# Optimization experiments

Measured on AMD Instinct MI355X. Metric: run time of the kernel, lower is better.

## Reference

```python
import jax, jax.numpy as jnp
import numpy as np

NEG_INF = -1e9

def setup_inputs() -> dict:
    key = jax.random.key(0)
    ks = jax.random.split(key, 7)
    B, NQ, NK, DQ, DK, DV, DH = 16, 128, 2048, 256, 256, 128, 64
    queries = jax.random.normal(ks[0], (B, NQ, DQ), dtype=jnp.float32)
    keys = jax.random.normal(ks[1], (B, NK, DK), dtype=jnp.float32)
    values = jax.random.normal(ks[2], (B, NK, DV), dtype=jnp.float32)
    valid_lens = jax.random.randint(ks[3], (B,), 1, NK + 1, dtype=jnp.int32)
    Wq = jax.random.normal(ks[4], (DQ, DH), dtype=jnp.float32) / np.sqrt(DQ)
    Wk = jax.random.normal(ks[5], (DK, DH), dtype=jnp.float32) / np.sqrt(DK)
    wv = jax.random.normal(ks[6], (DH,), dtype=jnp.float32) / np.sqrt(DH)
    return {"queries": queries, "keys": keys, "values": values,
            "valid_lens": valid_lens, "Wq": Wq, "Wk": Wk, "wv": wv}


def reference(queries, keys, values, valid_lens, Wq, Wk, wv):
    # Additive (Bahdanau) attention.
    q = jnp.einsum('bqd,dh->bqh', queries, Wq)   # [B, nq, dH]
    k = jnp.einsum('bkd,dh->bkh', keys, Wk)      # [B, nk, dH]
    # broadcast add -> tanh -> reduce with wv: scores [B, nq, nk]
    feat = jnp.tanh(q[:, :, None, :] + k[:, None, :, :])  # [B, nq, nk, dH]
    scores = jnp.einsum('bqkh,h->bqk', feat, wv)
    # masked softmax over nk using per-batch valid lengths
    nk = keys.shape[1]
    mask = jnp.arange(nk)[None, None, :] < valid_lens[:, None, None]  # [B,1,nk]
    scores = jnp.where(mask, scores, NEG_INF)
    attn = jax.nn.softmax(scores, axis=-1)
    # dropout is identity at eval time
    return jnp.einsum('bqk,bkv->bqv', attn, values)  # [B, nq, dv]
```

## Files before the change

### kernel.cpp

```cpp
#include <hip/hip_runtime.h>
#include <stddef.h>


__device__ __forceinline__ float fast_rcp(float x)  { return __builtin_amdgcn_rcpf(x); }
__device__ __forceinline__ float fast_exp2(float x) { return __builtin_amdgcn_exp2f(x); }

#define C2F 2.88539008177792681f
#define L2E 1.44269504088896340f

template<int MODE>
__device__ __forceinline__
void proj_body(const float* __restrict__ inb, const float* __restrict__ W,
               float* __restrict__ out, int b, int r0, int rowsPerB, int t)
{
  __shared__ float4 Wlds[256 * 16];
  __shared__ float  klds[64 * 36];

  const float4* W4 = (const float4*)W;
  #pragma unroll
  for (int i = 0; i < 16; ++i) Wlds[t + 256 * i] = W4[t + 256 * i];

  const int j = t >> 4;
  const int g = t & 15;

  float acc[4][4];
  #pragma unroll
  for (int m = 0; m < 4; ++m)
    acc[m][0] = acc[m][1] = acc[m][2] = acc[m][3] = 0.f;

  for (int dc = 0; dc < 8; ++dc) {
    {
      const int row = t >> 2, cs = (t & 3) * 8;
      const float* s = inb + row * 256 + dc * 32 + cs;
      float4 a0 = *(const float4*)s;
      float4 a1 = *(const float4*)(s + 4);
      float* dst = &klds[row * 36 + cs];
      *(float4*)dst       = a0;
      *(float4*)(dst + 4) = a1;
    }
    __syncthreads();
    #pragma unroll
    for (int d = 0; d < 32; ++d) {
      float4 w4 = Wlds[(dc * 32 + d) * 16 + j];
      #pragma unroll
      for (int m = 0; m < 4; ++m) {
        float kv = klds[(g + 16 * m) * 36 + d];
        acc[m][0] = fmaf(kv, w4.x, acc[m][0]);
        acc[m][1] = fmaf(kv, w4.y, acc[m][1]);
        acc[m][2] = fmaf(kv, w4.z, acc[m][2]);
        acc[m][3] = fmaf(kv, w4.w, acc[m][3]);
      }
    }
    __syncthreads();
  }

  if constexpr (MODE == 1) {
    #pragma unroll
    for (int m = 0; m < 4; ++m) {
      int k = r0 + g + 16 * m;
      size_t base = ((size_t)(b * 16 + (k >> 7)) * 64) * 128 + (k & 127);
      #pragma unroll
      for (int i = 0; i < 4; ++i)
        out[base + (size_t)(4 * j + i) * 128] = fast_exp2(C2F * acc[m][i]);
    }
  } else if constexpr (MODE == 2) {
    #pragma unroll
    for (int m = 0; m < 4; ++m) {
      int k = r0 + g + 16 * m;
      size_t base = (size_t)(b * 16 + (k >> 7)) * 8192 + (size_t)(k & 127) * 2;
      float e0 = fast_exp2(C2F * acc[m][0]);
      float e1 = fast_exp2(C2F * acc[m][1]);
      float e2 = fast_exp2(C2F * acc[m][2]);
      float e3 = fast_exp2(C2F * acc[m][3]);
      *(float2*)&out[base + (size_t)(2 * j) * 256]     = make_float2(e0, e1);
      *(float2*)&out[base + (size_t)(2 * j + 1) * 256] = make_float2(e2, e3);
    }
  } else {
    #pragma unroll
    for (int m = 0; m < 4; ++m) {
      int row = r0 + g + 16 * m;
      float4 o;
      o.x = fast_exp2(C2F * acc[m][0]);
      o.y = fast_exp2(C2F * acc[m][1]);
      o.z = fast_exp2(C2F * acc[m][2]);
      o.w = fast_exp2(C2F * acc[m][3]);
      *(float4*)&out[((size_t)b * rowsPerB + row) * 64 + 4 * j] = o;
    }
  }
}

__global__ __launch_bounds__(256)
void proj_qk_kernel(const float* __restrict__ queries, const float* __restrict__ keys,
                    const float* __restrict__ Wq, const float* __restrict__ Wk,
                    float* __restrict__ Eq, float* __restrict__ EkP,
                    const int* __restrict__ vlens)
{
  const int blk = blockIdx.x;
  if (blk >= 512) {
    const int idx = blk - 512;
    const int b = idx & 15, rt = idx >> 4, r0 = rt * 64;
    proj_body<0>(queries + ((size_t)b * 128 + r0) * 256, Wq, Eq, b, r0, 128,
                 threadIdx.x);
  } else {
    const int b = blk & 15, rt = blk >> 4, r0 = rt * 64;
    if (r0 >= vlens[b]) return;
    proj_body<2>(keys + ((size_t)b * 2048 + r0) * 256, Wk, EkP, b, r0, 2048,
                 threadIdx.x);
  }
}

template<int MODE, bool CHECK>
__global__ __launch_bounds__(256)
void proj_kernel(const float* __restrict__ in, const float* __restrict__ W,
                 float* __restrict__ out, const int* __restrict__ vlens,
                 int rowsPerB)
{
  const int t  = threadIdx.x;
  const int b  = blockIdx.x & 15;
  const int rt = blockIdx.x >> 4;
  const int r0 = rt * 64;
  if constexpr (CHECK) {
    if (r0 >= vlens[b]) return;
  }
  proj_body<MODE>(in + ((size_t)b * rowsPerB + r0) * 256, W, out, b, r0,
                  rowsPerB, t);
}

__global__ __launch_bounds__(512, 6)
void scorepv_kernel(const float* __restrict__ Eq, const float* __restrict__ EkP,
                    const float* __restrict__ values, const int* __restrict__ vlens,
                    const float* __restrict__ wv,
                    float* __restrict__ partial, float* __restrict__ tsum)
{
  const int blk = blockIdx.x;
  const int g   = blk >> 3;
  const int qq  = blk & 7;
  const int kt  = g >> 4;
  const int b   = g & 15;
  const int vl  = vlens[b];
  if (kt * 128 >= vl) return;

  __shared__ float ek_lds[64 * 128];

  const int t = threadIdx.x;

  {
    const float4* src = (const float4*)(EkP + (size_t)(b * 16 + kt) * 8192);
    float4* dst = (float4*)ek_lds;
    #pragma unroll
    for (int i = 0; i < 4; ++i) dst[t + 512 * i] = src[t + 512 * i];
  }

  float w0 = 0.f, W1 = 0.f;
  #pragma unroll
  for (int u = 0; u < 16; ++u) {
    float4 v = ((const float4*)wv)[u];
    w0 += v.x + v.y + v.z + v.w;
    W1 += fabsf(v.x) + fabsf(v.y) + fabsf(v.z) + fabsf(v.w);
  }

  __syncthreads();

  const int wave_u = __builtin_amdgcn_readfirstlane(t >> 6);
  const int lane   = t & 63;
  const int q0g    = qq * 16 + wave_u * 2;
  const int kp     = lane * 2;
  const float* eqb = Eq + (size_t)(b * 128 + q0g) * 64;

  float s[2][2] = {{w0, w0}, {w0, w0}};

  const float4* ek4 = (const float4*)ek_lds;
  #pragma unroll 8
  for (int hp = 0; hp < 32; ++hp) {
    float4 e = ek4[hp * 64 + lane];
    float2 wvp = *(const float2*)&wv[2 * hp];
    float wa = -2.0f * wvp.x, wb = -2.0f * wvp.y;
    #pragma unroll
    for (int q = 0; q < 2; ++q) {
      float2 eqp = *(const float2*)&eqb[q * 64 + 2 * hp];
      { float x0 = fmaf(eqp.x, e.x, 1.f), x1 = fmaf(eqp.y, e.y, 1.f);
        float y = fast_rcp(x0 * x1);
        float a = wb * x0; a = fmaf(wa, x1, a);
        s[q][0] = fmaf(a, y, s[q][0]); }
      { float x0 = fmaf(eqp.x, e.z, 1.f), x1 = fmaf(eqp.y, e.w, 1.f);
        float y = fast_rcp(x0 * x1);
        float a = wb * x0; a = fmaf(wa, x1, a);
        s[q][1] = fmaf(a, y, s[q][1]); }
    }
  }

  const int kbase = kt * 128 + kp;
  float p[2][2];
  #pragma unroll
  for (int q = 0; q < 2; ++q) {
    p[q][0] = (kbase     < vl) ? fast_exp2((s[q][0] - W1) * L2E) : 0.f;
    p[q][1] = (kbase + 1 < vl) ? fast_exp2((s[q][1] - W1) * L2E) : 0.f;
  }

  #pragma unroll
  for (int q = 0; q < 2; ++q) {
    float e = p[q][0] + p[q][1];
    #pragma unroll
    for (int m = 1; m < 64; m <<= 1) e += __shfl_xor(e, m, 64);
    if (lane == 0) tsum[(size_t)(b * 16 + kt) * 128 + q0g + q] = e;
  }

  __syncthreads();
  float* p_lds = ek_lds;
  const int q0l = wave_u * 2;
  *(float2*)&p_lds[kp * 20 + q0l]       = make_float2(p[0][0], p[1][0]);
  *(float2*)&p_lds[(kp + 1) * 20 + q0l] = make_float2(p[0][1], p[1][1]);
  __syncthreads();

  const int kg = t >> 7, v = t & 127;
  const int kloc = min(128, vl - kt * 128);
  const int k0 = kg * 32, k1 = min(k0 + 32, kloc);
  const int len = (k1 > k0) ? (k1 - k0) : 0;
  const int nfull = len & ~7;
  const float* vb = values + ((size_t)(b * 2048 + kt * 128)) * 128 + v;
  float acc[16];
  #pragma unroll
  for (int i = 0; i < 16; ++i) acc[i] = 0.f;

  for (int kb = k0; kb < k0 + nfull; kb += 8) {
    float vv[8];
    #pragma unroll
    for (int j = 0; j < 8; ++j) vv[j] = vb[(size_t)(kb + j) * 128];
    #pragma unroll
    for (int j = 0; j < 8; ++j) {
      const float* pr = &p_lds[(kb + j) * 20];
      float4 p0 = *(const float4*)&pr[0];
      float4 p1 = *(const float4*)&pr[4];
      float4 p2 = *(const float4*)&pr[8];
      float4 p3 = *(const float4*)&pr[12];
      float vx = vv[j];
      acc[ 0]=fmaf(p0.x,vx,acc[ 0]); acc[ 1]=fmaf(p0.y,vx,acc[ 1]);
      acc[ 2]=fmaf(p0.z,vx,acc[ 2]); acc[ 3]=fmaf(p0.w,vx,acc[ 3]);
      acc[ 4]=fmaf(p1.x,vx,acc[ 4]); acc[ 5]=fmaf(p1.y,vx,acc[ 5]);
      acc[ 6]=fmaf(p1.z,vx,acc[ 6]); acc[ 7]=fmaf(p1.w,vx,acc[ 7]);
      acc[ 8]=fmaf(p2.x,vx,acc[ 8]); acc[ 9]=fmaf(p2.y,vx,acc[ 9]);
      acc[10]=fmaf(p2.z,vx,acc[10]); acc[11]=fmaf(p2.w,vx,acc[11]);
      acc[12]=fmaf(p3.x,vx,acc[12]); acc[13]=fmaf(p3.y,vx,acc[13]);
      acc[14]=fmaf(p3.z,vx,acc[14]); acc[15]=fmaf(p3.w,vx,acc[15]);
    }
  }
  for (int k = k0 + nfull; k < k1; ++k) {
    float vx = vb[(size_t)k * 128];
    const float* pr = &p_lds[k * 20];
    #pragma unroll
    for (int q = 0; q < 16; ++q) acc[q] = fmaf(pr[q], vx, acc[q]);
  }

  __syncthreads();
  float* red = ek_lds;
  if (kg > 0) {
    #pragma unroll
    for (int q = 0; q < 16; ++q) red[(kg - 1) * 2048 + q * 128 + v] = acc[q];
  }
  __syncthreads();
  if (kg == 0) {
    #pragma unroll
    for (int q = 0; q < 16; ++q) {
      float tot = acc[q] + red[q * 128 + v] + red[2048 + q * 128 + v]
                + red[4096 + q * 128 + v];
      partial[(((size_t)(b * 128 + qq * 16 + q)) * 16 + kt) * 128 + v] = tot;
    }
  }
}

__global__ __launch_bounds__(256)
void reduce_kernel(const float* __restrict__ partial, const float* __restrict__ tsum,
                   const int* __restrict__ vlens, float* __restrict__ out)
{
  const int blk = blockIdx.x;
  const int b   = blk >> 6;
  const int q   = (blk & 63) * 2 + (threadIdx.x >> 7);
  const int v   = threadIdx.x & 127;
  const int ntk = (vlens[b] + 127) >> 7;

  float tot = 0.f;
  for (int i = 0; i < ntk; ++i)
    tot += tsum[(size_t)(b * 16 + i) * 128 + q];

  float acc = 0.f;
  const float* pp = partial + ((size_t)(b * 128 + q)) * 16 * 128 + v;
  for (int i = 0; i < ntk; ++i)
    acc += pp[(size_t)i * 128];

  out[((size_t)(b * 128 + q)) * 128 + v] = acc / tot;
}

__global__ __launch_bounds__(256)
void attn_kernel(const float* __restrict__ Eq, const float* __restrict__ EkT,
                 const float* __restrict__ values, const int* __restrict__ vlens,
                 const float* __restrict__ wv, float* __restrict__ out)
{
  const int t    = threadIdx.x;
  const int b    = blockIdx.x & 15;
  const int qt   = blockIdx.x >> 4;
  const int wave = t >> 6;
  const int lane = t & 63;

  __shared__ float4 sc4[512 * 4];
  __shared__ float  pvp[128 * 5];
  __shared__ float  linvs[4];

  const int vl = vlens[b];

  float eqv[64], wv2[64];
  float w0 = 0.f;
  {
    const float4* eq4 = (const float4*)(Eq + (size_t)(b * 128 + qt * 4 + wave) * 64);
    const float4* wv4 = (const float4*)wv;
    #pragma unroll
    for (int u = 0; u < 16; ++u) {
      float4 e = eq4[u], v = wv4[u];
      eqv[4*u+0] = e.x; eqv[4*u+1] = e.y; eqv[4*u+2] = e.z; eqv[4*u+3] = e.w;
      wv2[4*u+0] = -2.f * v.x; wv2[4*u+1] = -2.f * v.y;
      wv2[4*u+2] = -2.f * v.z; wv2[4*u+3] = -2.f * v.w;
      w0 += v.x + v.y + v.z + v.w;
    }
  }

  const int ktiles = (vl + 127) >> 7;
  const int kp = 2 * lane;
  for (int kt = 0; kt < ktiles; ++kt) {
    const float* tb = EkT + ((size_t)(b * 16 + kt) * 64) * 128 + kp;
    float s0 = w0, s1 = w0;
    #pragma unroll
    for (int h = 0; h < 64; ++h) {
      float2 ek = *(const float2*)(tb + (size_t)h * 128);
      float r0 = fast_rcp(fmaf(eqv[h], ek.x, 1.0f));
      float r1 = fast_rcp(fmaf(eqv[h], ek.y, 1.0f));
      s0 = fmaf(wv2[h], r0, s0);
      s1 = fmaf(wv2[h], r1, s1);
    }
    int k = kt * 128 + kp;
    if (k     >= vl) s0 = -1e9f;
    if (k + 1 >= vl) s1 = -1e9f;
    float* scf = (float*)sc4;
    *(float2*)(scf + (((k >> 2) * 4 + wave) * 4 + (k & 3))) = make_float2(s0, s1);
  }

  const int nq4 = (vl + 3) >> 2;
  float mx = -3e38f;
  for (int Q = lane; Q < nq4; Q += 64) {
    float4 f = sc4[Q * 4 + wave];
    mx = fmaxf(mx, fmaxf(fmaxf(f.x, f.y), fmaxf(f.z, f.w)));
  }
  #pragma unroll
  for (int msk = 1; msk < 64; msk <<= 1) mx = fmaxf(mx, __shfl_xor(mx, msk, 64));
  float lsum = 0.f;
  for (int Q = lane; Q < nq4; Q += 64) {
    float4 f = sc4[Q * 4 + wave];
    f.x = fast_exp2((f.x - mx) * L2E);
    f.y = fast_exp2((f.y - mx) * L2E);
    f.z = fast_exp2((f.z - mx) * L2E);
    f.w = fast_exp2((f.w - mx) * L2E);
    sc4[Q * 4 + wave] = f;
    lsum += f.x + f.y + f.z + f.w;
  }
  #pragma unroll
  for (int msk = 1; msk < 64; msk <<= 1) lsum += __shfl_xor(lsum, msk, 64);
  if (lane == 0) linvs[wave] = fast_rcp(lsum);
  __syncthreads();

  const int grp = t >> 7, v = t & 127;
  float acc[4] = {0.f, 0.f, 0.f, 0.f};
  const float* vb = values + (size_t)b * 2048 * 128 + v;
  for (int Q = grp; Q < nq4; Q += 2) {
    float4 p0 = sc4[Q * 4 + 0], p1 = sc4[Q * 4 + 1];
    float4 p2 = sc4[Q * 4 + 2], p3 = sc4[Q * 4 + 3];
    const float* vk = vb + (size_t)(Q * 4) * 128;
    float x;
    x = vk[0];
    acc[0]=fmaf(p0.x,x,acc[0]); acc[1]=fmaf(p1.x,x,acc[1]);
    acc[2]=fmaf(p2.x,x,acc[2]); acc[3]=fmaf(p3.x,x,acc[3]);
    x = vk[128];
    acc[0]=fmaf(p0.y,x,acc[0]); acc[1]=fmaf(p1.y,x,acc[1]);
    acc[2]=fmaf(p2.y,x,acc[2]); acc[3]=fmaf(p3.y,x,acc[3]);
    x = vk[256];
    acc[0]=fmaf(p0.z,x,acc[0]); acc[1]=fmaf(p1.z,x,acc[1]);
    acc[2]=fmaf(p2.z,x,acc[2]); acc[3]=fmaf(p3.z,x,acc[3]);
    x = vk[384];
    acc[0]=fmaf(p0.w,x,acc[0]); acc[1]=fmaf(p1.w,x,acc[1]);
    acc[2]=fmaf(p2.w,x,acc[2]); acc[3]=fmaf(p3.w,x,acc[3]);
  }
  if (grp == 1) {
    #pragma unroll
    for (int qq = 0; qq < 4; ++qq) pvp[v * 5 + qq] = acc[qq];
  }
  __syncthreads();
  if (grp == 0) {
    #pragma unroll
    for (int qq = 0; qq < 4; ++qq) {
      float tot = acc[qq] + pvp[v * 5 + qq];
      out[((size_t)(b * 128) + qt * 4 + qq) * 128 + v] = tot * linvs[qq];
    }
  }
}

extern "C" void kernel_launch(void* const* d_in, const int* in_sizes, int n_in,
                              void* d_out, int out_size, void* d_ws, size_t ws_size,
                              hipStream_t stream) {
  const float* queries = (const float*)d_in[0];
  const float* keys    = (const float*)d_in[1];
  const float* values  = (const float*)d_in[2];
  const int*   vlens   = (const int*)d_in[3];
  const float* Wq      = (const float*)d_in[4];
  const float* Wk      = (const float*)d_in[5];
  const float* wv      = (const float*)d_in[6];
  float* outp = (float*)d_out;

  float* base    = (float*)d_ws;
  float* Eq      = base;
  float* EkP     = base + 131072;
  float* tsumb   = base + 2228224;
  float* partial = base + 2260992;
  const size_t need = (size_t)(2260992 + 4194304) * 4;

  if (ws_size >= need) {
    hipLaunchKernelGGL(proj_qk_kernel, dim3(544), dim3(256), 0, stream,
                       queries, keys, Wq, Wk, Eq, EkP, vlens);
    hipLaunchKernelGGL(scorepv_kernel, dim3(2048), dim3(512), 0, stream,
                       Eq, EkP, values, vlens, wv, partial, tsumb);
    hipLaunchKernelGGL(reduce_kernel, dim3(1024), dim3(256), 0, stream,
                       partial, tsumb, vlens, outp);
  } else {
    hipLaunchKernelGGL((proj_kernel<0, false>), dim3(32), dim3(256), 0, stream,
                       queries, Wq, Eq, (const int*)nullptr, 128);
    hipLaunchKernelGGL((proj_kernel<1, true>), dim3(512), dim3(256), 0, stream,
                       keys, Wk, EkP, vlens, 2048);
    hipLaunchKernelGGL(attn_kernel, dim3(512), dim3(256), 0, stream,
                       Eq, EkP, values, vlens, wv, outp);
  }
}
```

Measured before the change: 91.24 us.

## Use persistent blocks with atomic work queue over valid tiles only

Adds an init kernel that builds prefix sums of per-batch valid tile counts and resets atomic counters. The projection and score/PV kernels become persistent loops that pull compacted work units from an atomic counter, so no blocks are launched only to exit on masked tiles. The score kernel's launch bounds occupancy hint is raised from 6 to 8. This costs an extra tiny kernel launch, per-unit atomics and barriers, and a linear batch search per unit.

```diff
diff --git a/kernel.cpp b/kernel.cpp
--- a/kernel.cpp
+++ b/kernel.cpp
@@ -7,6 +7,32 @@
 
 #define C2F 2.88539008177792681f
 #define L2E 1.44269504088896340f
+
+#define M_CNTP 0
+#define M_CNTS 1
+#define M_NP   2
+#define M_NS   3
+#define M_PPK  8
+#define M_PSC  32
+
+__global__ void init_kernel(const int* __restrict__ vlens, int* __restrict__ meta)
+{
+  if (threadIdx.x == 0) {
+    int ap = 0, as = 0;
+    meta[M_PPK] = 0; meta[M_PSC] = 0;
+    for (int b = 0; b < 16; ++b) {
+      int vl = vlens[b];
+      ap += (vl + 63) >> 6;
+      as += (vl + 127) >> 7;
+      meta[M_PPK + 1 + b] = ap;
+      meta[M_PSC + 1 + b] = as;
+    }
+    meta[M_NP]   = 32 + ap;
+    meta[M_NS]   = as * 8;
+    meta[M_CNTP] = 0;
+    meta[M_CNTS] = 0;
+  }
+}
 
 template<int MODE>
 __device__ __forceinline__
@@ -93,19 +119,28 @@
 void proj_qk_kernel(const float* __restrict__ queries, const float* __restrict__ keys,
                     const float* __restrict__ Wq, const float* __restrict__ Wk,
                     float* __restrict__ Eq, float* __restrict__ EkP,
-                    const int* __restrict__ vlens)
-{
-  const int blk = blockIdx.x;
-  if (blk >= 512) {
-    const int idx = blk - 512;
-    const int b = idx & 15, rt = idx >> 4, r0 = rt * 64;
-    proj_body<0>(queries + ((size_t)b * 128 + r0) * 256, Wq, Eq, b, r0, 128,
-                 threadIdx.x);
-  } else {
-    const int b = blk & 15, rt = blk >> 4, r0 = rt * 64;
-    if (r0 >= vlens[b]) return;
-    proj_body<2>(keys + ((size_t)b * 2048 + r0) * 256, Wk, EkP, b, r0, 2048,
-                 threadIdx.x);
+                    int* __restrict__ meta)
+{
+  __shared__ int sh_u;
+  const int t = threadIdx.x;
+  const int nunits = meta[M_NP];
+  for (;;) {
+    __syncthreads();
+    if (t == 0) sh_u = atomicAdd(&meta[M_CNTP], 1);
+    __syncthreads();
+    const int u = sh_u;
+    if (u >= nunits) break;
+    if (u < 32) {
+      const int b = u & 15, rt = u >> 4, r0 = rt * 64;
+      proj_body<0>(queries + ((size_t)b * 128 + r0) * 256, Wq, Eq, b, r0, 128, t);
+    } else {
+      int w = u - 32;
+      int b = 0;
+      while (w >= meta[M_PPK + 1 + b]) ++b;
+      const int rt = w - meta[M_PPK + b];
+      const int r0 = rt * 64;
+      proj_body<2>(keys + ((size_t)b * 2048 + r0) * 256, Wk, EkP, b, r0, 2048, t);
+    }
   }
 }
 
@@ -126,30 +161,18 @@
                   rowsPerB, t);
 }
 
-__global__ __launch_bounds__(512, 6)
+__global__ __launch_bounds__(512, 8)
 void scorepv_kernel(const float* __restrict__ Eq, const float* __restrict__ EkP,
                     const float* __restrict__ values, const int* __restrict__ vlens,
                     const float* __restrict__ wv,
-                    float* __restrict__ partial, float* __restrict__ tsum)
-{
-  const int blk = blockIdx.x;
-  const int g   = blk >> 3;
-  const int qq  = blk & 7;
-  const int kt  = g >> 4;
-  const int b   = g & 15;
-  const int vl  = vlens[b];
-  if (kt * 128 >= vl) return;
-
+                    float* __restrict__ partial, float* __restrict__ tsum,
+                    int* __restrict__ meta)
+{
   __shared__ float ek_lds[64 * 128];
+  __shared__ int sh_u;
 
   const int t = threadIdx.x;
-
-  {
-    const float4* src = (const float4*)(EkP + (size_t)(b * 16 + kt) * 8192);
-    float4* dst = (float4*)ek_lds;
-    #pragma unroll
-    for (int i = 0; i < 4; ++i) dst[t + 512 * i] = src[t + 512 * i];
-  }
+  const int nunits = meta[M_NS];
 
   float w0 = 0.f, W1 = 0.f;
   #pragma unroll
@@ -159,111 +182,132 @@
     W1 += fabsf(v.x) + fabsf(v.y) + fabsf(v.z) + fabsf(v.w);
   }
 
-  __syncthreads();
-
-  const int wave_u = __builtin_amdgcn_readfirstlane(t >> 6);
-  const int lane   = t & 63;
-  const int q0g    = qq * 16 + wave_u * 2;
-  const int kp     = lane * 2;
-  const float* eqb = Eq + (size_t)(b * 128 + q0g) * 64;
-
-  float s[2][2] = {{w0, w0}, {w0, w0}};
-
-  const float4* ek4 = (const float4*)ek_lds;
-  #pragma unroll 8
-  for (int hp = 0; hp < 32; ++hp) {
-    float4 e = ek4[hp * 64 + lane];
-    float2 wvp = *(const float2*)&wv[2 * hp];
-    float wa = -2.0f * wvp.x, wb = -2.0f * wvp.y;
+  for (;;) {
+    __syncthreads();
+    if (t == 0) sh_u = atomicAdd(&meta[M_CNTS], 1);
+    __syncthreads();
+    const int u = sh_u;
+    if (u >= nunits) break;
+
+    const int w  = u >> 3;
+    const int qq = u & 7;
+    int b = 0;
+    while (w >= meta[M_PSC + 1 + b]) ++b;
+    const int kt = w - meta[M_PSC + b];
+    const int vl = vlens[b];
+
+    {
+      const float4* src = (const float4*)(EkP + (size_t)(b * 16 + kt) * 8192);
+      float4* dst = (float4*)ek_lds;
+      #pragma unroll
+      for (int i = 0; i < 4; ++i) dst[t + 512 * i] = src[t + 512 * i];
+    }
+    __syncthreads();
+
+    const int wave_u = __builtin_amdgcn_readfirstlane(t >> 6);
+    const int lane   = t & 63;
+    const int q0g    = qq * 16 + wave_u * 2;
+    const int kp     = lane * 2;
+    const float* eqb = Eq + (size_t)(b * 128 + q0g) * 64;
+
+    float s[2][2] = {{w0, w0}, {w0, w0}};
+
+    const float4* ek4 = (const float4*)ek_lds;
+    #pragma unroll 8
+    for (int hp = 0; hp < 32; ++hp) {
+      float4 e = ek4[hp * 64 + lane];
+      float2 wvp = *(const float2*)&wv[2 * hp];
+      float wa = -2.0f * wvp.x, wb = -2.0f * wvp.y;
+      #pragma unroll
+      for (int q = 0; q < 2; ++q) {
+        float2 eqp = *(const float2*)&eqb[q * 64 + 2 * hp];
+        { float x0 = fmaf(eqp.x, e.x, 1.f), x1 = fmaf(eqp.y, e.y, 1.f);
+          float y = fast_rcp(x0 * x1);
+          float a = wb * x0; a = fmaf(wa, x1, a);
+          s[q][0] = fmaf(a, y, s[q][0]); }
+        { float x0 = fmaf(eqp.x, e.z, 1.f), x1 = fmaf(eqp.y, e.w, 1.f);
+          float y = fast_rcp(x0 * x1);
+          float a = wb * x0; a = fmaf(wa, x1, a);
+          s[q][1] = fmaf(a, y, s[q][1]); }
+      }
+    }
+
+    const int kbase = kt * 128 + kp;
+    float p[2][2];
     #pragma unroll
     for (int q = 0; q < 2; ++q) {
-      float2 eqp = *(const float2*)&eqb[q * 64 + 2 * hp];
-      { float x0 = fmaf(eqp.x, e.x, 1.f), x1 = fmaf(eqp.y, e.y, 1.f);
-        float y = fast_rcp(x0 * x1);
-        float a = wb * x0; a = fmaf(wa, x1, a);
-        s[q][0] = fmaf(a, y, s[q][0]); }
-      { float x0 = fmaf(eqp.x, e.z, 1.f), x1 = fmaf(eqp.y, e.w, 1.f);
-        float y = fast_rcp(x0 * x1);
-        float a = wb * x0; a = fmaf(wa, x1, a);
-        s[q][1] = fmaf(a, y, s[q][1]); }
-    }
-  }
-
-  const int kbase = kt * 128 + kp;
-  float p[2][2];
-  #pragma unroll
-  for (int q = 0; q < 2; ++q) {
-    p[q][0] = (kbase     < vl) ? fast_exp2((s[q][0] - W1) * L2E) : 0.f;
-    p[q][1] = (kbase + 1 < vl) ? fast_exp2((s[q][1] - W1) * L2E) : 0.f;
-  }
-
-  #pragma unroll
-  for (int q = 0; q < 2; ++q) {
-    float e = p[q][0] + p[q][1];
-    #pragma unroll
-    for (int m = 1; m < 64; m <<= 1) e += __shfl_xor(e, m, 64);
-    if (lane == 0) tsum[(size_t)(b * 16 + kt) * 128 + q0g + q] = e;
-  }
-
-  __syncthreads();
-  float* p_lds = ek_lds;
-  const int q0l = wave_u * 2;
-  *(float2*)&p_lds[kp * 20 + q0l]       = make_float2(p[0][0], p[1][0]);
-  *(float2*)&p_lds[(kp + 1) * 20 + q0l] = make_float2(p[0][1], p[1][1]);
-  __syncthreads();
-
-  const int kg = t >> 7, v = t & 127;
-  const int kloc = min(128, vl - kt * 128);
-  const int k0 = kg * 32, k1 = min(k0 + 32, kloc);
-  const int len = (k1 > k0) ? (k1 - k0) : 0;
-  const int nfull = len & ~7;
-  const float* vb = values + ((size_t)(b * 2048 + kt * 128)) * 128 + v;
-  float acc[16];
-  #pragma unroll
-  for (int i = 0; i < 16; ++i) acc[i] = 0.f;
-
-  for (int kb = k0; kb < k0 + nfull; kb += 8) {
-    float vv[8];
-    #pragma unroll
-    for (int j = 0; j < 8; ++j) vv[j] = vb[(size_t)(kb + j) * 128];
-    #pragma unroll
-    for (int j = 0; j < 8; ++j) {
-      const float* pr = &p_lds[(kb + j) * 20];
-      float4 p0 = *(const float4*)&pr[0];
-      float4 p1 = *(const float4*)&pr[4];
-      float4 p2 = *(const float4*)&pr[8];
-      float4 p3 = *(const float4*)&pr[12];
-      float vx = vv[j];
-      acc[ 0]=fmaf(p0.x,vx,acc[ 0]); acc[ 1]=fmaf(p0.y,vx,acc[ 1]);
-      acc[ 2]=fmaf(p0.z,vx,acc[ 2]); acc[ 3]=fmaf(p0.w,vx,acc[ 3]);
-      acc[ 4]=fmaf(p1.x,vx,acc[ 4]); acc[ 5]=fmaf(p1.y,vx,acc[ 5]);
-      acc[ 6]=fmaf(p1.z,vx,acc[ 6]); acc[ 7]=fmaf(p1.w,vx,acc[ 7]);
-      acc[ 8]=fmaf(p2.x,vx,acc[ 8]); acc[ 9]=fmaf(p2.y,vx,acc[ 9]);
-      acc[10]=fmaf(p2.z,vx,acc[10]); acc[11]=fmaf(p2.w,vx,acc[11]);
-      acc[12]=fmaf(p3.x,vx,acc[12]); acc[13]=fmaf(p3.y,vx,acc[13]);
-      acc[14]=fmaf(p3.z,vx,acc[14]); acc[15]=fmaf(p3.w,vx,acc[15]);
-    }
-  }
-  for (int k = k0 + nfull; k < k1; ++k) {
-    float vx = vb[(size_t)k * 128];
-    const float* pr = &p_lds[k * 20];
-    #pragma unroll
-    for (int q = 0; q < 16; ++q) acc[q] = fmaf(pr[q], vx, acc[q]);
-  }
-
-  __syncthreads();
-  float* red = ek_lds;
-  if (kg > 0) {
-    #pragma unroll
-    for (int q = 0; q < 16; ++q) red[(kg - 1) * 2048 + q * 128 + v] = acc[q];
-  }
-  __syncthreads();
-  if (kg == 0) {
-    #pragma unroll
-    for (int q = 0; q < 16; ++q) {
-      float tot = acc[q] + red[q * 128 + v] + red[2048 + q * 128 + v]
-                + red[4096 + q * 128 + v];
-      partial[(((size_t)(b * 128 + qq * 16 + q)) * 16 + kt) * 128 + v] = tot;
+      p[q][0] = (kbase     < vl) ? fast_exp2((s[q][0] - W1) * L2E) : 0.f;
+      p[q][1] = (kbase + 1 < vl) ? fast_exp2((s[q][1] - W1) * L2E) : 0.f;
+    }
+
+    #pragma unroll
+    for (int q = 0; q < 2; ++q) {
+      float e = p[q][0] + p[q][1];
+      #pragma unroll
+      for (int m = 1; m < 64; m <<= 1) e += __shfl_xor(e, m, 64);
+      if (lane == 0) tsum[(size_t)(b * 16 + kt) * 128 + q0g + q] = e;
+    }
+
+    __syncthreads();
+    float* p_lds = ek_lds;
+    const int q0l = wave_u * 2;
+    *(float2*)&p_lds[kp * 20 + q0l]       = make_float2(p[0][0], p[1][0]);
+    *(float2*)&p_lds[(kp + 1) * 20 + q0l] = make_float2(p[0][1], p[1][1]);
+    __syncthreads();
+
+    const int kg = t >> 7, v = t & 127;
+    const int kloc = min(128, vl - kt * 128);
+    const int k0 = kg * 32, k1 = min(k0 + 32, kloc);
+    const int len = (k1 > k0) ? (k1 - k0) : 0;
+    const int nfull = len & ~7;
+    const float* vb = values + ((size_t)(b * 2048 + kt * 128)) * 128 + v;
+    float acc[16];
+    #pragma unroll
+    for (int i = 0; i < 16; ++i) acc[i] = 0.f;
+
+    for (int kb = k0; kb < k0 + nfull; kb += 8) {
+      float vv[8];
+      #pragma unroll
+      for (int j = 0; j < 8; ++j) vv[j] = vb[(size_t)(kb + j) * 128];
+      #pragma unroll
+      for (int j = 0; j < 8; ++j) {
+        const float* pr = &p_lds[(kb + j) * 20];
+        float4 p0 = *(const float4*)&pr[0];
+        float4 p1 = *(const float4*)&pr[4];
+        float4 p2 = *(const float4*)&pr[8];
+        float4 p3 = *(const float4*)&pr[12];
+        float vx = vv[j];
+        acc[ 0]=fmaf(p0.x,vx,acc[ 0]); acc[ 1]=fmaf(p0.y,vx,acc[ 1]);
+        acc[ 2]=fmaf(p0.z,vx,acc[ 2]); acc[ 3]=fmaf(p0.w,vx,acc[ 3]);
+        acc[ 4]=fmaf(p1.x,vx,acc[ 4]); acc[ 5]=fmaf(p1.y,vx,acc[ 5]);
+        acc[ 6]=fmaf(p1.z,vx,acc[ 6]); acc[ 7]=fmaf(p1.w,vx,acc[ 7]);
+        acc[ 8]=fmaf(p2.x,vx,acc[ 8]); acc[ 9]=fmaf(p2.y,vx,acc[ 9]);
+        acc[10]=fmaf(p2.z,vx,acc[10]); acc[11]=fmaf(p2.w,vx,acc[11]);
+        acc[12]=fmaf(p3.x,vx,acc[12]); acc[13]=fmaf(p3.y,vx,acc[13]);
+        acc[14]=fmaf(p3.z,vx,acc[14]); acc[15]=fmaf(p3.w,vx,acc[15]);
+      }
+    }
+    for (int k = k0 + nfull; k < k1; ++k) {
+      float vx = vb[(size_t)k * 128];
+      const float* pr = &p_lds[k * 20];
+      #pragma unroll
+      for (int q = 0; q < 16; ++q) acc[q] = fmaf(pr[q], vx, acc[q]);
+    }
+
+    __syncthreads();
+    float* red = ek_lds;
+    if (kg > 0) {
+      #pragma unroll
+      for (int q = 0; q < 16; ++q) red[(kg - 1) * 2048 + q * 128 + v] = acc[q];
+    }
+    __syncthreads();
+    if (kg == 0) {
+      #pragma unroll
+      for (int q = 0; q < 16; ++q) {
+        float tot = acc[q] + red[q * 128 + v] + red[2048 + q * 128 + v]
+                  + red[4096 + q * 128 + v];
+        partial[(((size_t)(b * 128 + qq * 16 + q)) * 16 + kt) * 128 + v] = tot;
+      }
     }
   }
 }
@@ -417,13 +461,15 @@
   float* EkP     = base + 131072;
   float* tsumb   = base + 2228224;
   float* partial = base + 2260992;
-  const size_t need = (size_t)(2260992 + 4194304) * 4;
+  int*   meta    = (int*)(base + 6455296);
+  const size_t need = (size_t)6455296 * 4 + 64 * 4;
 
   if (ws_size >= need) {
-    hipLaunchKernelGGL(proj_qk_kernel, dim3(544), dim3(256), 0, stream,
-                       queries, keys, Wq, Wk, Eq, EkP, vlens);
-    hipLaunchKernelGGL(scorepv_kernel, dim3(2048), dim3(512), 0, stream,
-                       Eq, EkP, values, vlens, wv, partial, tsumb);
+    hipLaunchKernelGGL(init_kernel, dim3(1), dim3(64), 0, stream, vlens, meta);
+    hipLaunchKernelGGL(proj_qk_kernel, dim3(512), dim3(256), 0, stream,
+                       queries, keys, Wq, Wk, Eq, EkP, meta);
+    hipLaunchKernelGGL(scorepv_kernel, dim3(1024), dim3(512), 0, stream,
+                       Eq, EkP, values, vlens, wv, partial, tsumb, meta);
     hipLaunchKernelGGL(reduce_kernel, dim3(1024), dim3(256), 0, stream,
                        partial, tsumb, vlens, outp);
   } else {
```

After: 90.32 us. About the same (-1.0%).

## Use persistent work-queue scheduling for score/PV kernel with packed Eq+wv layout

Applied to the files above, without the earlier changes.

Adds an init kernel that computes per-batch prefix sums of active key tiles, and turns scorepv into a persistent kernel of 768 blocks that pull compacted work units through an atomic counter. This avoids launching and early-exiting idle blocks for masked tiles and balances load. The query projection now writes Eq interleaved with -2*wv into a float4 layout, which is staged in LDS so the inner loop needs fewer global loads. The cost is an extra kernel launch, serialized atomic fetches with extra barriers per unit, and a larger workspace requirement.

```diff
diff --git a/kernel.cpp b/kernel.cpp
--- a/kernel.cpp
+++ b/kernel.cpp
@@ -7,11 +7,30 @@
 
 #define C2F 2.88539008177792681f
 #define L2E 1.44269504088896340f
+
+#define M_CNTS 0
+#define M_NS   1
+#define M_PSC  32
+
+__global__ void init_kernel(const int* __restrict__ vlens, int* __restrict__ meta)
+{
+  if (threadIdx.x == 0) {
+    int as = 0;
+    meta[M_PSC] = 0;
+    for (int b = 0; b < 16; ++b) {
+      as += (vlens[b] + 127) >> 7;
+      meta[M_PSC + 1 + b] = as;
+    }
+    meta[M_NS]   = as * 8;
+    meta[M_CNTS] = 0;
+  }
+}
 
 template<int MODE>
 __device__ __forceinline__
 void proj_body(const float* __restrict__ inb, const float* __restrict__ W,
-               float* __restrict__ out, int b, int r0, int rowsPerB, int t)
+               float* __restrict__ out, const float* __restrict__ wv,
+               int b, int r0, int rowsPerB, int t)
 {
   __shared__ float4 Wlds[256 * 16];
   __shared__ float  klds[64 * 36];
@@ -75,6 +94,19 @@
       *(float2*)&out[base + (size_t)(2 * j) * 256]     = make_float2(e0, e1);
       *(float2*)&out[base + (size_t)(2 * j + 1) * 256] = make_float2(e2, e3);
     }
+  } else if constexpr (MODE == 3) {
+    float4 wq = ((const float4*)wv)[j];
+    #pragma unroll
+    for (int m = 0; m < 4; ++m) {
+      int row = r0 + g + 16 * m;
+      float e0 = fast_exp2(C2F * acc[m][0]);
+      float e1 = fast_exp2(C2F * acc[m][1]);
+      float e2 = fast_exp2(C2F * acc[m][2]);
+      float e3 = fast_exp2(C2F * acc[m][3]);
+      float4* dst = (float4*)out + ((size_t)(b * 128 + row)) * 32;
+      dst[2 * j]     = make_float4(e0, e1, -2.f * wq.x, -2.f * wq.y);
+      dst[2 * j + 1] = make_float4(e2, e3, -2.f * wq.z, -2.f * wq.w);
+    }
   } else {
     #pragma unroll
     for (int m = 0; m < 4; ++m) {
@@ -92,19 +124,19 @@
 __global__ __launch_bounds__(256)
 void proj_qk_kernel(const float* __restrict__ queries, const float* __restrict__ keys,
                     const float* __restrict__ Wq, const float* __restrict__ Wk,
-                    float* __restrict__ Eq, float* __restrict__ EkP,
-                    const int* __restrict__ vlens)
+                    float* __restrict__ EqW, float* __restrict__ EkP,
+                    const float* __restrict__ wv, const int* __restrict__ vlens)
 {
   const int blk = blockIdx.x;
   if (blk >= 512) {
     const int idx = blk - 512;
     const int b = idx & 15, rt = idx >> 4, r0 = rt * 64;
-    proj_body<0>(queries + ((size_t)b * 128 + r0) * 256, Wq, Eq, b, r0, 128,
+    proj_body<3>(queries + ((size_t)b * 128 + r0) * 256, Wq, EqW, wv, b, r0, 128,
                  threadIdx.x);
   } else {
     const int b = blk & 15, rt = blk >> 4, r0 = rt * 64;
     if (r0 >= vlens[b]) return;
-    proj_body<2>(keys + ((size_t)b * 2048 + r0) * 256, Wk, EkP, b, r0, 2048,
+    proj_body<2>(keys + ((size_t)b * 2048 + r0) * 256, Wk, EkP, wv, b, r0, 2048,
                  threadIdx.x);
   }
 }
@@ -122,36 +154,26 @@
   if constexpr (CHECK) {
     if (r0 >= vlens[b]) return;
   }
-  proj_body<MODE>(in + ((size_t)b * rowsPerB + r0) * 256, W, out, b, r0,
-                  rowsPerB, t);
+  proj_body<MODE>(in + ((size_t)b * rowsPerB + r0) * 256, W, out,
+                  (const float*)nullptr, b, r0, rowsPerB, t);
 }
 
 __global__ __launch_bounds__(512, 6)
-void scorepv_kernel(const float* __restrict__ Eq, const float* __restrict__ EkP,
+void scorepv_kernel(const float* __restrict__ EqW, const float* __restrict__ EkP,
                     const float* __restrict__ values, const int* __restrict__ vlens,
                     const float* __restrict__ wv,
-                    float* __restrict__ partial, float* __restrict__ tsum)
-{
-  const int blk = blockIdx.x;
-  const int g   = blk >> 3;
-  const int qq  = blk & 7;
-  const int kt  = g >> 4;
-  const int b   = g & 15;
-  const int vl  = vlens[b];
-  if (kt * 128 >= vl) return;
-
-  __shared__ float ek_lds[64 * 128];
+                    float* __restrict__ partial, float* __restrict__ tsum,
+                    int* __restrict__ meta)
+{
+  __shared__ float ek_lds[8192];
+  __shared__ float p_lds[128 * 20];
+  __shared__ int sh_u, sh_pre[17];
 
   const int t = threadIdx.x;
-
-  {
-    const float4* src = (const float4*)(EkP + (size_t)(b * 16 + kt) * 8192);
-    float4* dst = (float4*)ek_lds;
-    #pragma unroll
-    for (int i = 0; i < 4; ++i) dst[t + 512 * i] = src[t + 512 * i];
-  }
-
-  float w0 = 0.f, W1 = 0.f;
+  if (t < 17) sh_pre[t] = meta[M_PSC + t];
+  const int nunits = meta[M_NS];
+
+  float W1 = 0.f, w0 = 0.f;
   #pragma unroll
   for (int u = 0; u < 16; ++u) {
     float4 v = ((const float4*)wv)[u];
@@ -159,111 +181,130 @@
     W1 += fabsf(v.x) + fabsf(v.y) + fabsf(v.z) + fabsf(v.w);
   }
 
-  __syncthreads();
-
   const int wave_u = __builtin_amdgcn_readfirstlane(t >> 6);
   const int lane   = t & 63;
-  const int q0g    = qq * 16 + wave_u * 2;
   const int kp     = lane * 2;
-  const float* eqb = Eq + (size_t)(b * 128 + q0g) * 64;
-
-  float s[2][2] = {{w0, w0}, {w0, w0}};
-
-  const float4* ek4 = (const float4*)ek_lds;
-  #pragma unroll 8
-  for (int hp = 0; hp < 32; ++hp) {
-    float4 e = ek4[hp * 64 + lane];
-    float2 wvp = *(const float2*)&wv[2 * hp];
-    float wa = -2.0f * wvp.x, wb = -2.0f * wvp.y;
+  const int q0l    = wave_u * 2;
+
+  for (;;) {
+    __syncthreads();
+    if (t == 0) sh_u = atomicAdd(&meta[M_CNTS], 1);
+    __syncthreads();
+    const int u = sh_u;
+    if (u >= nunits) break;
+
+    const int w  = u >> 3;
+    const int qq = u & 7;
+    int b = 0;
+    while (w >= sh_pre[1 + b]) ++b;
+    const int kt = w - sh_pre[b];
+    const int vl = vlens[b];
+
+    {
+      const float4* src = (const float4*)(EkP + (size_t)(b * 16 + kt) * 8192);
+      float4* dst = (float4*)ek_lds;
+      #pragma unroll
+      for (int i = 0; i < 4; ++i) dst[t + 512 * i] = src[t + 512 * i];
+      const float4* qsrc = (const float4*)EqW + ((size_t)(b * 128 + qq * 16)) * 32;
+      ((float4*)p_lds)[t] = qsrc[t];
+    }
+    __syncthreads();
+
+    float s[2][2] = {{w0, w0}, {w0, w0}};
+    const float4* ek4 = (const float4*)ek_lds;
+    const float4* eqw = (const float4*)p_lds;
+    #pragma unroll 8
+    for (int hp = 0; hp < 32; ++hp) {
+      float4 e = ek4[hp * 64 + lane];
+      #pragma unroll
+      for (int q = 0; q < 2; ++q) {
+        float4 ew = eqw[(q0l + q) * 32 + hp];
+        { float x0 = fmaf(ew.x, e.x, 1.f), x1 = fmaf(ew.y, e.y, 1.f);
+          float y = fast_rcp(x0 * x1);
+          float a = ew.w * x0; a = fmaf(ew.z, x1, a);
+          s[q][0] = fmaf(a, y, s[q][0]); }
+        { float x0 = fmaf(ew.x, e.z, 1.f), x1 = fmaf(ew.y, e.w, 1.f);
+          float y = fast_rcp(x0 * x1);
+          float a = ew.w * x0; a = fmaf(ew.z, x1, a);
+          s[q][1] = fmaf(a, y, s[q][1]); }
+      }
+    }
+
+    const int kbase = kt * 128 + kp;
+    float p[2][2];
     #pragma unroll
     for (int q = 0; q < 2; ++q) {
-      float2 eqp = *(const float2*)&eqb[q * 64 + 2 * hp];
-      { float x0 = fmaf(eqp.x, e.x, 1.f), x1 = fmaf(eqp.y, e.y, 1.f);
-        float y = fast_rcp(x0 * x1);
-        float a = wb * x0; a = fmaf(wa, x1, a);
-        s[q][0] = fmaf(a, y, s[q][0]); }
-      { float x0 = fmaf(eqp.x, e.z, 1.f), x1 = fmaf(eqp.y, e.w, 1.f);
-        float y = fast_rcp(x0 * x1);
-        float a = wb * x0; a = fmaf(wa, x1, a);
-        s[q][1] = fmaf(a, y, s[q][1]); }
-    }
-  }
-
-  const int kbase = kt * 128 + kp;
-  float p[2][2];
-  #pragma unroll
-  for (int q = 0; q < 2; ++q) {
-    p[q][0] = (kbase     < vl) ? fast_exp2((s[q][0] - W1) * L2E) : 0.f;
-    p[q][1] = (kbase + 1 < vl) ? fast_exp2((s[q][1] - W1) * L2E) : 0.f;
-  }
-
-  #pragma unroll
-  for (int q = 0; q < 2; ++q) {
-    float e = p[q][0] + p[q][1];
-    #pragma unroll
-    for (int m = 1; m < 64; m <<= 1) e += __shfl_xor(e, m, 64);
-    if (lane == 0) tsum[(size_t)(b * 16 + kt) * 128 + q0g + q] = e;
-  }
-
-  __syncthreads();
-  float* p_lds = ek_lds;
-  const int q0l = wave_u * 2;
-  *(float2*)&p_lds[kp * 20 + q0l]       = make_float2(p[0][0], p[1][0]);
-  *(float2*)&p_lds[(kp + 1) * 20 + q0l] = make_float2(p[0][1], p[1][1]);
-  __syncthreads();
-
-  const int kg = t >> 7, v = t & 127;
-  const int kloc = min(128, vl - kt * 128);
-  const int k0 = kg * 32, k1 = min(k0 + 32, kloc);
-  const int len = (k1 > k0) ? (k1 - k0) : 0;
-  const int nfull = len & ~7;
-  const float* vb = values + ((size_t)(b * 2048 + kt * 128)) * 128 + v;
-  float acc[16];
-  #pragma unroll
-  for (int i = 0; i < 16; ++i) acc[i] = 0.f;
-
-  for (int kb = k0; kb < k0 + nfull; kb += 8) {
-    float vv[8];
-    #pragma unroll
-    for (int j = 0; j < 8; ++j) vv[j] = vb[(size_t)(kb + j) * 128];
-    #pragma unroll
-    for (int j = 0; j < 8; ++j) {
-      const float* pr = &p_lds[(kb + j) * 20];
-      float4 p0 = *(const float4*)&pr[0];
-      float4 p1 = *(const float4*)&pr[4];
-      float4 p2 = *(const float4*)&pr[8];
-      float4 p3 = *(const float4*)&pr[12];
-      float vx = vv[j];
-      acc[ 0]=fmaf(p0.x,vx,acc[ 0]); acc[ 1]=fmaf(p0.y,vx,acc[ 1]);
-      acc[ 2]=fmaf(p0.z,vx,acc[ 2]); acc[ 3]=fmaf(p0.w,vx,acc[ 3]);
-      acc[ 4]=fmaf(p1.x,vx,acc[ 4]); acc[ 5]=fmaf(p1.y,vx,acc[ 5]);
-      acc[ 6]=fmaf(p1.z,vx,acc[ 6]); acc[ 7]=fmaf(p1.w,vx,acc[ 7]);
-      acc[ 8]=fmaf(p2.x,vx,acc[ 8]); acc[ 9]=fmaf(p2.y,vx,acc[ 9]);
-      acc[10]=fmaf(p2.z,vx,acc[10]); acc[11]=fmaf(p2.w,vx,acc[11]);
-      acc[12]=fmaf(p3.x,vx,acc[12]); acc[13]=fmaf(p3.y,vx,acc[13]);
-      acc[14]=fmaf(p3.z,vx,acc[14]); acc[15]=fmaf(p3.w,vx,acc[15]);
-    }
-  }
-  for (int k = k0 + nfull; k < k1; ++k) {
-    float vx = vb[(size_t)k * 128];
-    const float* pr = &p_lds[k * 20];
-    #pragma unroll
-    for (int q = 0; q < 16; ++q) acc[q] = fmaf(pr[q], vx, acc[q]);
-  }
-
-  __syncthreads();
-  float* red = ek_lds;
-  if (kg > 0) {
-    #pragma unroll
-    for (int q = 0; q < 16; ++q) red[(kg - 1) * 2048 + q * 128 + v] = acc[q];
-  }
-  __syncthreads();
-  if (kg == 0) {
-    #pragma unroll
-    for (int q = 0; q < 16; ++q) {
-      float tot = acc[q] + red[q * 128 + v] + red[2048 + q * 128 + v]
-                + red[4096 + q * 128 + v];
-      partial[(((size_t)(b * 128 + qq * 16 + q)) * 16 + kt) * 128 + v] = tot;
+      p[q][0] = (kbase     < vl) ? fast_exp2((s[q][0] - W1) * L2E) : 0.f;
+      p[q][1] = (kbase + 1 < vl) ? fast_exp2((s[q][1] - W1) * L2E) : 0.f;
+    }
+
+    const int q0g = qq * 16 + q0l;
+    #pragma unroll
+    for (int q = 0; q < 2; ++q) {
+      float e = p[q][0] + p[q][1];
+      #pragma unroll
+      for (int m = 1; m < 64; m <<= 1) e += __shfl_xor(e, m, 64);
+      if (lane == 0) tsum[(size_t)(b * 16 + kt) * 128 + q0g + q] = e;
+    }
+
+    __syncthreads();
+    *(float2*)&p_lds[kp * 20 + q0l]       = make_float2(p[0][0], p[1][0]);
+    *(float2*)&p_lds[(kp + 1) * 20 + q0l] = make_float2(p[0][1], p[1][1]);
+    __syncthreads();
+
+    const int kg = t >> 7, v = t & 127;
+    const int kloc = min(128, vl - kt * 128);
+    const int k0 = kg * 32, k1 = min(k0 + 32, kloc);
+    const int len = (k1 > k0) ? (k1 - k0) : 0;
+    const int nfull = len & ~7;
+    const float* vb = values + ((size_t)(b * 2048 + kt * 128)) * 128 + v;
+    float acc[16];
+    #pragma unroll
+    for (int i = 0; i < 16; ++i) acc[i] = 0.f;
+
+    for (int kb = k0; kb < k0 + nfull; kb += 8) {
+      float vv[8];
+      #pragma unroll
+      for (int j = 0; j < 8; ++j) vv[j] = vb[(size_t)(kb + j) * 128];
+      #pragma unroll
+      for (int j = 0; j < 8; ++j) {
+        const float* pr = &p_lds[(kb + j) * 20];
+        float4 p0 = *(const float4*)&pr[0];
+        float4 p1 = *(const float4*)&pr[4];
+        float4 p2 = *(const float4*)&pr[8];
+        float4 p3 = *(const float4*)&pr[12];
+        float vx = vv[j];
+        acc[ 0]=fmaf(p0.x,vx,acc[ 0]); acc[ 1]=fmaf(p0.y,vx,acc[ 1]);
+        acc[ 2]=fmaf(p0.z,vx,acc[ 2]); acc[ 3]=fmaf(p0.w,vx,acc[ 3]);
+        acc[ 4]=fmaf(p1.x,vx,acc[ 4]); acc[ 5]=fmaf(p1.y,vx,acc[ 5]);
+        acc[ 6]=fmaf(p1.z,vx,acc[ 6]); acc[ 7]=fmaf(p1.w,vx,acc[ 7]);
+        acc[ 8]=fmaf(p2.x,vx,acc[ 8]); acc[ 9]=fmaf(p2.y,vx,acc[ 9]);
+        acc[10]=fmaf(p2.z,vx,acc[10]); acc[11]=fmaf(p2.w,vx,acc[11]);
+        acc[12]=fmaf(p3.x,vx,acc[12]); acc[13]=fmaf(p3.y,vx,acc[13]);
+        acc[14]=fmaf(p3.z,vx,acc[14]); acc[15]=fmaf(p3.w,vx,acc[15]);
+      }
+    }
+    for (int k = k0 + nfull; k < k1; ++k) {
+      float vx = vb[(size_t)k * 128];
+      const float* pr = &p_lds[k * 20];
+      #pragma unroll
+      for (int q = 0; q < 16; ++q) acc[q] = fmaf(pr[q], vx, acc[q]);
+    }
+
+    __syncthreads();
+    float* red = ek_lds;
+    if (kg > 0) {
+      #pragma unroll
+      for (int q = 0; q < 16; ++q) red[(kg - 1) * 2048 + q * 128 + v] = acc[q];
+    }
+    __syncthreads();
+    if (kg == 0) {
+      #pragma unroll
+      for (int q = 0; q < 16; ++q) {
+        float tot = acc[q] + red[q * 128 + v] + red[2048 + q * 128 + v]
+                  + red[4096 + q * 128 + v];
+        partial[(((size_t)(b * 128 + qq * 16 + q)) * 16 + kt) * 128 + v] = tot;
+      }
     }
   }
 }
@@ -413,25 +454,27 @@
   float* outp = (float*)d_out;
 
   float* base    = (float*)d_ws;
-  float* Eq      = base;
-  float* EkP     = base + 131072;
-  float* tsumb   = base + 2228224;
-  float* partial = base + 2260992;
-  const size_t need = (size_t)(2260992 + 4194304) * 4;
+  float* EqW     = base;
+  float* EkP     = base + 262144;
+  float* tsumb   = base + 2359296;
+  float* partial = base + 2392064;
+  int*   meta    = (int*)(base + 6586368);
+  const size_t need = (size_t)6586368 * 4 + 256;
 
   if (ws_size >= need) {
+    hipLaunchKernelGGL(init_kernel, dim3(1), dim3(64), 0, stream, vlens, meta);
     hipLaunchKernelGGL(proj_qk_kernel, dim3(544), dim3(256), 0, stream,
-                       queries, keys, Wq, Wk, Eq, EkP, vlens);
-    hipLaunchKernelGGL(scorepv_kernel, dim3(2048), dim3(512), 0, stream,
-                       Eq, EkP, values, vlens, wv, partial, tsumb);
+                       queries, keys, Wq, Wk, EqW, EkP, wv, vlens);
+    hipLaunchKernelGGL(scorepv_kernel, dim3(768), dim3(512), 0, stream,
+                       EqW, EkP, values, vlens, wv, partial, tsumb, meta);
     hipLaunchKernelGGL(reduce_kernel, dim3(1024), dim3(256), 0, stream,
                        partial, tsumb, vlens, outp);
   } else {
     hipLaunchKernelGGL((proj_kernel<0, false>), dim3(32), dim3(256), 0, stream,
-                       queries, Wq, Eq, (const int*)nullptr, 128);
+                       queries, Wq, EqW, (const int*)nullptr, 128);
     hipLaunchKernelGGL((proj_kernel<1, true>), dim3(512), dim3(256), 0, stream,
                        keys, Wk, EkP, vlens, 2048);
     hipLaunchKernelGGL(attn_kernel, dim3(512), dim3(256), 0, stream,
-                       Eq, EkP, values, vlens, wv, outp);
-  }
-}
+                       EqW, EkP, values, vlens, wv, outp);
+  }
+}
```

Result: faster. 84.79 us (-7.1%).
